# Kernel tuning notes

Measured on AMD Instinct MI355X. Metric: run time of the kernel, lower is better.

## Reference

```python
import jax, jax.numpy as jnp
import numpy as np

B, T, C, H = 4, 2048, 1024, 16
HD = C // H


def setup_inputs() -> dict:
    key = jax.random.key(0)
    k1, k2, k3, k4 = jax.random.split(key, 4)
    x = jax.random.normal(k1, (B, T, C), dtype=jnp.float32)
    pad_mask = jnp.ones((B, T), dtype=jnp.int32)
    # Linear weights stored as (in, out); torch Linear uses W.T so math is identical.
    w_attn = jax.random.normal(k2, (C, 3 * C), dtype=jnp.float32) * (1.0 / np.sqrt(C))
    w_proj = jax.random.normal(k3, (C, C), dtype=jnp.float32) * (1.0 / np.sqrt(C))
    b_proj = jax.random.normal(k4, (C,), dtype=jnp.float32) * 0.01
    return {"x": x, "pad_mask": pad_mask, "w_attn": w_attn, "w_proj": w_proj, "b_proj": b_proj}


def reference(x, pad_mask, w_attn, w_proj, b_proj):
    Bx, Tx, Cx = x.shape
    hd = Cx // H
    qkv = x @ w_attn                                  # (B,T,3C)
    q, k, v = jnp.split(qkv, 3, axis=2)
    # (B,T,C) -> (B,H,T,hd)
    q = q.reshape(Bx, Tx, H, hd).transpose(0, 2, 1, 3)
    k = k.reshape(Bx, Tx, H, hd).transpose(0, 2, 1, 3)
    v = v.reshape(Bx, Tx, H, hd).transpose(0, 2, 1, 3)
    att = jnp.einsum('bhqd,bhkd->bhqk', q, k) * (1.0 / np.sqrt(hd))
    causal = jnp.tril(jnp.ones((Tx, Tx), dtype=bool))[None, None]       # (1,1,T,T)
    keep = causal & (pad_mask[:, None, None, :] != 0)                   # (B,1,T,T) broadcast
    att = jnp.where(keep, att, -jnp.inf)
    att = jax.nn.softmax(att, axis=-1)
    # dropout p=0.0 (eval) -> identity
    y = jnp.einsum('bhqk,bhkd->bhqd', att, v)
    y = y.transpose(0, 2, 1, 3).reshape(Bx, Tx, Cx)
    return y @ w_proj + b_proj
```

## Files before the change

kernel.cpp:

```cpp
#include <hip/hip_runtime.h>
#include <hip/hip_bf16.h>


using short8  = __attribute__((ext_vector_type(8))) short;
using float4_ = __attribute__((ext_vector_type(4))) float;

#define Bb   4
#define Tt   2048
#define Cc   1024
#define Hh   16
#define HDd  64

__device__ __forceinline__ float bf2f(unsigned short u) {
    union { float f; unsigned int i; } x; x.i = ((unsigned int)u) << 16; return x.f;
}
__device__ __forceinline__ unsigned short f2bf(float f) {
    union { float f; unsigned int i; } x; x.f = f;
    unsigned int r = x.i + 0x7fff + ((x.i >> 16) & 1);
    return (unsigned short)(r >> 16);
}
__device__ __forceinline__ float4_ bmfma(short8 a, short8 b, float4_ c) {
    return __builtin_amdgcn_mfma_f32_16x16x32_bf16(a, b, c, 0, 0, 0);
}
__device__ __forceinline__ void gl2lds16(const unsigned short* g, unsigned short* l) {
    __builtin_amdgcn_global_load_lds(
        (const __attribute__((address_space(1))) void*)g,
        (__attribute__((address_space(3))) void*)l, 16, 0, 0);
}

__global__ __launch_bounds__(256) void convert_f32_bf16(
    const float* __restrict__ in, unsigned short* __restrict__ out)
{
    size_t idx = ((size_t)blockIdx.x * 256 + threadIdx.x) * 8;
    float4_ f0 = *(const float4_*)&in[idx];
    float4_ f1 = *(const float4_*)&in[idx + 4];
    short8 h;
    h[0] = (short)f2bf(f0[0]); h[1] = (short)f2bf(f0[1]);
    h[2] = (short)f2bf(f0[2]); h[3] = (short)f2bf(f0[3]);
    h[4] = (short)f2bf(f1[0]); h[5] = (short)f2bf(f1[1]);
    h[6] = (short)f2bf(f1[2]); h[7] = (short)f2bf(f1[3]);
    *(short8*)&out[idx] = h;
}

__global__ __launch_bounds__(256) void transpose_f32_bf16(
    const float* __restrict__ in, unsigned short* __restrict__ out,
    int R, int Ccols)
{
    __shared__ unsigned short tile[32][33];
    int c0 = blockIdx.x * 32, r0 = blockIdx.y * 32;
    int tx = threadIdx.x & 31, ty = threadIdx.x >> 5;
    for (int o = 0; o < 32; o += 8)
        tile[ty + o][tx] = f2bf(in[(size_t)(r0 + ty + o) * Ccols + c0 + tx]);
    __syncthreads();
    for (int o = 0; o < 32; o += 8)
        out[(size_t)(c0 + ty + o) * R + r0 + tx] = tile[tx][ty + o];
}

#define GBK 64

__device__ __forceinline__ void gemm128_main(
    const unsigned short* __restrict__ A, const unsigned short* __restrict__ Bt,
    int K, int m0, int n0,
    unsigned short* As, unsigned short* Bs, float4_ acc[4][4])
{
    int tid  = threadIdx.x;
    int wave = tid >> 6, lane = tid & 63;
    int wm = (wave >> 1) * 64, wn = (wave & 1) * 64;
    int lr = lane & 15, lg = lane >> 4;
    int srow = tid >> 3;
    int scol = (tid & 7) * 8;

    for (int k0 = 0; k0 < K; k0 += GBK) {
        #pragma unroll
        for (int j = 0; j < 4; j++) {
            int row = j * 32 + srow;
            gl2lds16(&A [(size_t)(m0 + row) * K + k0 + scol], &As[row * GBK + scol]);
            gl2lds16(&Bt[(size_t)(n0 + row) * K + k0 + scol], &Bs[row * GBK + scol]);
        }
        __syncthreads();
        #pragma unroll
        for (int ks = 0; ks < GBK; ks += 32) {
            short8 af[4], bf[4];
            #pragma unroll
            for (int i = 0; i < 4; i++) {
                af[i] = *(const short8*)&As[(wm + i * 16 + lr) * GBK + ks + lg * 8];
                bf[i] = *(const short8*)&Bs[(wn + i * 16 + lr) * GBK + ks + lg * 8];
            }
            #pragma unroll
            for (int i = 0; i < 4; i++)
                #pragma unroll
                for (int j = 0; j < 4; j++)
                    acc[i][j] = bmfma(af[i], bf[j], acc[i][j]);
        }
        __syncthreads();
    }
}

__global__ __launch_bounds__(256) void gemm_qkv(
    const unsigned short* __restrict__ A,
    const unsigned short* __restrict__ Bt,
    unsigned short* __restrict__ Q,
    unsigned short* __restrict__ Ko,
    unsigned short* __restrict__ V)
{
    __shared__ unsigned short As[128 * GBK];
    __shared__ unsigned short Bs[128 * GBK];
    int m0 = blockIdx.x * 128, n0 = blockIdx.y * 128;
    float4_ acc[4][4] = {};
    gemm128_main(A, Bt, 1024, m0, n0, As, Bs, acc);

    int lane = threadIdx.x & 63, wave = threadIdx.x >> 6;
    int wm = (wave >> 1) * 64, wn = (wave & 1) * 64;
    int lr = lane & 15, lg = lane >> 4;
    #pragma unroll
    for (int i = 0; i < 4; i++)
        #pragma unroll
        for (int j = 0; j < 4; j++) {
            int n = n0 + wn + 16 * j + lr;
            int which = n >> 10;
            int c = n & 1023;
            int h = c >> 6, d = c & 63;
            unsigned short* dst = (which == 0) ? Q : ((which == 1) ? Ko : V);
            float sc2 = (which == 0) ? 0.125f : 1.0f;
            #pragma unroll
            for (int r = 0; r < 4; r++) {
                int m = m0 + wm + 16 * i + lg * 4 + r;
                int b = m >> 11, t = m & 2047;
                dst[(((size_t)(b * Hh + h) * Tt) + t) * HDd + d] = f2bf(acc[i][j][r] * sc2);
            }
        }
}

__global__ __launch_bounds__(256) void gemm_proj(
    const unsigned short* __restrict__ A,
    const unsigned short* __restrict__ Bt,
    const float* __restrict__ bias,
    float* __restrict__ Out)
{
    __shared__ unsigned short As[128 * GBK];
    __shared__ unsigned short Bs[128 * GBK];
    int m0 = blockIdx.x * 128, n0 = blockIdx.y * 128;
    float4_ acc[4][4] = {};
    gemm128_main(A, Bt, 1024, m0, n0, As, Bs, acc);

    int lane = threadIdx.x & 63, wave = threadIdx.x >> 6;
    int wm = (wave >> 1) * 64, wn = (wave & 1) * 64;
    int lr = lane & 15, lg = lane >> 4;
    #pragma unroll
    for (int i = 0; i < 4; i++)
        #pragma unroll
        for (int j = 0; j < 4; j++) {
            int n = n0 + wn + 16 * j + lr;
            float bv = bias[n];
            #pragma unroll
            for (int r = 0; r < 4; r++) {
                int m = m0 + wm + 16 * i + lg * 4 + r;
                Out[(size_t)m * 1024 + n] = acc[i][j][r] + bv;
            }
        }
}

#define DPAD 72

__global__ __launch_bounds__(256) void attn_fwd(
    const unsigned short* __restrict__ Q,
    const unsigned short* __restrict__ Kg,
    const unsigned short* __restrict__ Vg,
    const int* __restrict__ pad,
    unsigned short* __restrict__ Y)
{
    __shared__ unsigned short smem[128 * DPAD];
    unsigned short* Kt = smem;
    unsigned short* Vt = smem + 64 * DPAD;

    int flat = blockIdx.x;
    int qb = 31 - (flat >> 6);
    int bh = flat & 63;
    int b  = bh >> 4, h = bh & 15;
    const size_t base = (size_t)bh * Tt * HDd;
    int tid  = threadIdx.x;
    int wave = tid >> 6, lane = tid & 63;
    int lr = lane & 15, lg = lane >> 4;
    int q0 = qb * 64 + wave * 16;
    unsigned short* Pw = &Kt[wave * 16 * DPAD];
    const int* padRow = pad + b * Tt;

    short8 qf0 = *(const short8*)&Q[base + (size_t)(q0 + lr) * HDd + lg * 8];
    short8 qf1 = *(const short8*)&Q[base + (size_t)(q0 + lr) * HDd + 32 + lg * 8];

    float m_i[4], l_i[4];
    float4_ o_acc[4];
    #pragma unroll
    for (int r = 0; r < 4; r++) { m_i[r] = -1e30f; l_i[r] = 0.f; }
    #pragma unroll
    for (int dt = 0; dt < 4; dt++) o_acc[dt] = (float4_){0.f, 0.f, 0.f, 0.f};

    for (int kt = 0; kt <= qb; kt++) {
        int k0 = kt * 64;
        {
            int r = tid >> 2, cbase = (tid & 3) * 8;
            #pragma unroll
            for (int half = 0; half < 2; half++) {
                int c = cbase + half * 32;
                *(short8*)&Kt[r * DPAD + c] =
                    *(const short8*)&Kg[base + (size_t)(k0 + r) * HDd + c];
                alignas(16) unsigned short tmp[8];
                *(short8*)tmp = *(const short8*)&Vg[base + (size_t)(k0 + r) * HDd + c];
                #pragma unroll
                for (int j = 0; j < 8; j++) {
                    int d = c + j;
                    Vt[d * DPAD + ((((r >> 3) ^ (d >> 3)) << 3) | (r & 7))] = tmp[j];
                }
            }
        }
        __syncthreads();

        float4_ s[4];
        #pragma unroll
        for (int nt = 0; nt < 4; nt++) {
            short8 kf0 = *(const short8*)&Kt[(nt * 16 + lr) * DPAD + lg * 8];
            short8 kf1 = *(const short8*)&Kt[(nt * 16 + lr) * DPAD + 32 + lg * 8];
            float4_ a = (float4_){0.f, 0.f, 0.f, 0.f};
            a = bmfma(qf0, kf0, a);
            a = bmfma(qf1, kf1, a);
            s[nt] = a;
        }
        #pragma unroll
        for (int nt = 0; nt < 4; nt++) {
            int key = k0 + nt * 16 + lr;
            bool keep_k = padRow[key] != 0;
            #pragma unroll
            for (int r = 0; r < 4; r++) {
                int qrow = q0 + lg * 4 + r;
                float sv = s[nt][r];
                if (!keep_k || key > qrow) sv = -1e30f;
                s[nt][r] = sv;
            }
        }
        float mn[4], alpha[4];
        #pragma unroll
        for (int r = 0; r < 4; r++) {
            float v = fmaxf(fmaxf(s[0][r], s[1][r]), fmaxf(s[2][r], s[3][r]));
            #pragma unroll
            for (int off = 1; off < 16; off <<= 1)
                v = fmaxf(v, __shfl_xor(v, off, 64));
            float m_new = fmaxf(m_i[r], v);
            alpha[r] = __expf(m_i[r] - m_new);
            mn[r] = m_new;
        }
        float rsum[4] = {0.f, 0.f, 0.f, 0.f};
        #pragma unroll
        for (int nt = 0; nt < 4; nt++)
            #pragma unroll
            for (int r = 0; r < 4; r++) {
                float p = __expf(s[nt][r] - mn[r]);
                s[nt][r] = p;
                rsum[r] += p;
            }
        #pragma unroll
        for (int r = 0; r < 4; r++) {
            float v = rsum[r];
            #pragma unroll
            for (int off = 1; off < 16; off <<= 1)
                v += __shfl_xor(v, off, 64);
            l_i[r] = l_i[r] * alpha[r] + v;
            m_i[r] = mn[r];
        }

        __syncthreads();

        #pragma unroll
        for (int nt = 0; nt < 4; nt++)
            #pragma unroll
            for (int r = 0; r < 4; r++)
                Pw[(lg * 4 + r) * DPAD + nt * 16 + lr] = f2bf(s[nt][r]);
        #pragma unroll
        for (int dt = 0; dt < 4; dt++)
            #pragma unroll
            for (int r = 0; r < 4; r++)
                o_acc[dt][r] *= alpha[r];
        short8 pf0 = *(const short8*)&Pw[lr * DPAD + lg * 8];
        short8 pf1 = *(const short8*)&Pw[lr * DPAD + 32 + lg * 8];
        #pragma unroll
        for (int dt = 0; dt < 4; dt++) {
            int d = dt * 16 + lr;
            short8 vf0 = *(const short8*)&Vt[d * DPAD + ((lg ^ (d >> 3)) << 3)];
            short8 vf1 = *(const short8*)&Vt[d * DPAD + (((lg + 4) ^ (d >> 3)) << 3)];
            o_acc[dt] = bmfma(pf0, vf0, o_acc[dt]);
            o_acc[dt] = bmfma(pf1, vf1, o_acc[dt]);
        }
        __syncthreads();
    }

    #pragma unroll
    for (int dt = 0; dt < 4; dt++)
        #pragma unroll
        for (int r = 0; r < 4; r++) {
            int qrow = q0 + lg * 4 + r;
            Y[((size_t)b * Tt + qrow) * Cc + h * HDd + dt * 16 + lr] =
                f2bf(o_acc[dt][r] / l_i[r]);
        }
}

extern "C" void kernel_launch(void* const* d_in, const int* in_sizes, int n_in,
                              void* d_out, int out_size, void* d_ws, size_t ws_size,
                              hipStream_t stream)
{
    const float* x      = (const float*)d_in[0];
    const int*   pad    = (const int*)d_in[1];
    const float* w_attn = (const float*)d_in[2];
    const float* w_proj = (const float*)d_in[3];
    const float* b_proj = (const float*)d_in[4];
    float*       out    = (float*)d_out;

    unsigned short* Wta = (unsigned short*)d_ws;
    unsigned short* Wtp = Wta + (size_t)3072 * 1024;
    unsigned short* Xb  = Wtp + (size_t)1024 * 1024;
    unsigned short* Yb  = Xb;
    unsigned short* Qb  = Xb + (size_t)8192 * 1024;
    unsigned short* Kb  = Qb + (size_t)Bb * Hh * Tt * HDd;
    unsigned short* Vb  = Kb + (size_t)Bb * Hh * Tt * HDd;

    convert_f32_bf16<<<dim3(4096), 256, 0, stream>>>(x, Xb);
    transpose_f32_bf16<<<dim3(3072 / 32, 1024 / 32), 256, 0, stream>>>(w_attn, Wta, 1024, 3072);
    transpose_f32_bf16<<<dim3(1024 / 32, 1024 / 32), 256, 0, stream>>>(w_proj, Wtp, 1024, 1024);
    gemm_qkv<<<dim3(8192 / 128, 3072 / 128), 256, 0, stream>>>(Xb, Wta, Qb, Kb, Vb);
    attn_fwd<<<dim3(2048), 256, 0, stream>>>(Qb, Kb, Vb, pad, Yb);
    gemm_proj<<<dim3(8192 / 128, 1024 / 128), 256, 0, stream>>>(Yb, Wtp, b_proj, out);
}
```

Measured before the change: 331.5 us.

## Pair causal query blocks per workgroup, use exp2 softmax, skip interior masking

```diff
diff --git a/kernel.cpp b/kernel.cpp
--- a/kernel.cpp
+++ b/kernel.cpp
@@ -10,6 +10,8 @@
 #define Cc   1024
 #define Hh   16
 #define HDd  64
+
+#define EXP2F(x) __builtin_amdgcn_exp2f(x)
 
 __device__ __forceinline__ float bf2f(unsigned short u) {
     union { float f; unsigned int i; } x; x.i = ((unsigned int)u) << 16; return x.f;
@@ -96,6 +98,8 @@
     }
 }
 
+#define QSCALE 0.180336879f
+
 __global__ __launch_bounds__(256) void gemm_qkv(
     const unsigned short* __restrict__ A,
     const unsigned short* __restrict__ Bt,
@@ -121,7 +125,7 @@
             int c = n & 1023;
             int h = c >> 6, d = c & 63;
             unsigned short* dst = (which == 0) ? Q : ((which == 1) ? Ko : V);
-            float sc2 = (which == 0) ? 0.125f : 1.0f;
+            float sc2 = (which == 0) ? QSCALE : 1.0f;
             #pragma unroll
             for (int r = 0; r < 4; r++) {
                 int m = m0 + wm + 16 * i + lg * 4 + r;
@@ -162,40 +166,131 @@
 
 #define DPAD 72
 
-__global__ __launch_bounds__(256) void attn_fwd(
+#define ATTN_TILE(q0X, qX0, qX1, mX, lX, oX)                                   \
+    {                                                                          \
+        float4_ s[4];                                                          \
+        _Pragma("unroll")                                                      \
+        for (int nt = 0; nt < 4; nt++) {                                       \
+            short8 kf0 = *(const short8*)&Kt[(nt * 16 + lr) * DPAD + lg * 8];  \
+            short8 kf1 = *(const short8*)&Kt[(nt * 16 + lr) * DPAD + 32 + lg * 8]; \
+            float4_ a = (float4_){0.f, 0.f, 0.f, 0.f};                         \
+            a = bmfma(qX0, kf0, a);                                            \
+            a = bmfma(qX1, kf1, a);                                            \
+            s[nt] = a;                                                         \
+        }                                                                      \
+        bool interior = (k0 + 63 <= (q0X));                                    \
+        if (interior) {                                                        \
+            _Pragma("unroll")                                                  \
+            for (int nt = 0; nt < 4; nt++) {                                   \
+                _Pragma("unroll")                                              \
+                for (int r = 0; r < 4; r++) s[nt][r] += pmask[nt];             \
+            }                                                                  \
+        } else {                                                               \
+            _Pragma("unroll")                                                  \
+            for (int nt = 0; nt < 4; nt++) {                                   \
+                int key = k0 + nt * 16 + lr;                                   \
+                _Pragma("unroll")                                              \
+                for (int r = 0; r < 4; r++) {                                  \
+                    int qrow = (q0X) + lg * 4 + r;                             \
+                    float sv = s[nt][r] + pmask[nt];                           \
+                    if (key > qrow) sv = -1e30f;                               \
+                    s[nt][r] = sv;                                             \
+                }                                                              \
+            }                                                                  \
+        }                                                                      \
+        float mn[4], alpha[4];                                                 \
+        _Pragma("unroll")                                                      \
+        for (int r = 0; r < 4; r++) {                                          \
+            float v = fmaxf(fmaxf(s[0][r], s[1][r]), fmaxf(s[2][r], s[3][r])); \
+            _Pragma("unroll")                                                  \
+            for (int off = 1; off < 16; off <<= 1)                             \
+                v = fmaxf(v, __shfl_xor(v, off, 64));                          \
+            float m_new = fmaxf(mX[r], v);                                     \
+            alpha[r] = EXP2F(mX[r] - m_new);                                   \
+            mn[r] = m_new;                                                     \
+        }                                                                      \
+        float rsum[4] = {0.f, 0.f, 0.f, 0.f};                                  \
+        _Pragma("unroll")                                                      \
+        for (int nt = 0; nt < 4; nt++)                                         \
+            _Pragma("unroll")                                                  \
+            for (int r = 0; r < 4; r++) {                                      \
+                float p = EXP2F(s[nt][r] - mn[r]);                             \
+                s[nt][r] = p;                                                  \
+                rsum[r] += p;                                                  \
+            }                                                                  \
+        _Pragma("unroll")                                                      \
+        for (int r = 0; r < 4; r++) {                                          \
+            float v = rsum[r];                                                 \
+            _Pragma("unroll")                                                  \
+            for (int off = 1; off < 16; off <<= 1)                             \
+                v += __shfl_xor(v, off, 64);                                   \
+            lX[r] = lX[r] * alpha[r] + v;                                      \
+            mX[r] = mn[r];                                                     \
+        }                                                                      \
+        _Pragma("unroll")                                                      \
+        for (int nt = 0; nt < 4; nt++)                                         \
+            _Pragma("unroll")                                                  \
+            for (int r = 0; r < 4; r++)                                        \
+                Pw[(lg * 4 + r) * DPAD + nt * 16 + lr] = f2bf(s[nt][r]);       \
+        _Pragma("unroll")                                                      \
+        for (int dt = 0; dt < 4; dt++)                                         \
+            _Pragma("unroll")                                                  \
+            for (int r = 0; r < 4; r++)                                        \
+                oX[dt][r] *= alpha[r];                                         \
+        short8 pf0 = *(const short8*)&Pw[lr * DPAD + lg * 8];                  \
+        short8 pf1 = *(const short8*)&Pw[lr * DPAD + 32 + lg * 8];             \
+        _Pragma("unroll")                                                      \
+        for (int dt = 0; dt < 4; dt++) {                                       \
+            int d = dt * 16 + lr;                                              \
+            short8 vf0 = *(const short8*)&Vt[d * DPAD + ((lg ^ (d >> 3)) << 3)];       \
+            short8 vf1 = *(const short8*)&Vt[d * DPAD + (((lg + 4) ^ (d >> 3)) << 3)]; \
+            oX[dt] = bmfma(pf0, vf0, oX[dt]);                                  \
+            oX[dt] = bmfma(pf1, vf1, oX[dt]);                                  \
+        }                                                                      \
+    }
+
+__global__ __launch_bounds__(256, 4) void attn_fwd(
     const unsigned short* __restrict__ Q,
     const unsigned short* __restrict__ Kg,
     const unsigned short* __restrict__ Vg,
     const int* __restrict__ pad,
     unsigned short* __restrict__ Y)
 {
-    __shared__ unsigned short smem[128 * DPAD];
+    __shared__ unsigned short smem[192 * DPAD];
     unsigned short* Kt = smem;
     unsigned short* Vt = smem + 64 * DPAD;
-
-    int flat = blockIdx.x;
-    int qb = 31 - (flat >> 6);
-    int bh = flat & 63;
+    unsigned short* Pl = smem + 128 * DPAD;
+
+    int qpair = blockIdx.x;
+    int bh = blockIdx.y;
     int b  = bh >> 4, h = bh & 15;
     const size_t base = (size_t)bh * Tt * HDd;
     int tid  = threadIdx.x;
     int wave = tid >> 6, lane = tid & 63;
     int lr = lane & 15, lg = lane >> 4;
-    int q0 = qb * 64 + wave * 16;
-    unsigned short* Pw = &Kt[wave * 16 * DPAD];
+    unsigned short* Pw = &Pl[wave * 16 * DPAD];
     const int* padRow = pad + b * Tt;
 
-    short8 qf0 = *(const short8*)&Q[base + (size_t)(q0 + lr) * HDd + lg * 8];
-    short8 qf1 = *(const short8*)&Q[base + (size_t)(q0 + lr) * HDd + 32 + lg * 8];
-
-    float m_i[4], l_i[4];
-    float4_ o_acc[4];
-    #pragma unroll
-    for (int r = 0; r < 4; r++) { m_i[r] = -1e30f; l_i[r] = 0.f; }
-    #pragma unroll
-    for (int dt = 0; dt < 4; dt++) o_acc[dt] = (float4_){0.f, 0.f, 0.f, 0.f};
-
-    for (int kt = 0; kt <= qb; kt++) {
+    int qbA = qpair, qbB = 31 - qpair;
+    int q0A = qbA * 64 + wave * 16;
+    int q0B = qbB * 64 + wave * 16;
+
+    short8 qfA0 = *(const short8*)&Q[base + (size_t)(q0A + lr) * HDd + lg * 8];
+    short8 qfA1 = *(const short8*)&Q[base + (size_t)(q0A + lr) * HDd + 32 + lg * 8];
+    short8 qfB0 = *(const short8*)&Q[base + (size_t)(q0B + lr) * HDd + lg * 8];
+    short8 qfB1 = *(const short8*)&Q[base + (size_t)(q0B + lr) * HDd + 32 + lg * 8];
+
+    float mA[4], lA[4], mB[4], lB[4];
+    float4_ oA[4], oB[4];
+    #pragma unroll
+    for (int r = 0; r < 4; r++) { mA[r] = -1e30f; lA[r] = 0.f; mB[r] = -1e30f; lB[r] = 0.f; }
+    #pragma unroll
+    for (int dt = 0; dt < 4; dt++) {
+        oA[dt] = (float4_){0.f, 0.f, 0.f, 0.f};
+        oB[dt] = (float4_){0.f, 0.f, 0.f, 0.f};
+    }
+
+    for (int kt = 0; kt <= qbB; kt++) {
         int k0 = kt * 64;
         {
             int r = tid >> 2, cbase = (tid & 3) * 8;
@@ -215,80 +310,15 @@
         }
         __syncthreads();
 
-        float4_ s[4];
-        #pragma unroll
-        for (int nt = 0; nt < 4; nt++) {
-            short8 kf0 = *(const short8*)&Kt[(nt * 16 + lr) * DPAD + lg * 8];
-            short8 kf1 = *(const short8*)&Kt[(nt * 16 + lr) * DPAD + 32 + lg * 8];
-            float4_ a = (float4_){0.f, 0.f, 0.f, 0.f};
-            a = bmfma(qf0, kf0, a);
-            a = bmfma(qf1, kf1, a);
-            s[nt] = a;
-        }
-        #pragma unroll
-        for (int nt = 0; nt < 4; nt++) {
-            int key = k0 + nt * 16 + lr;
-            bool keep_k = padRow[key] != 0;
-            #pragma unroll
-            for (int r = 0; r < 4; r++) {
-                int qrow = q0 + lg * 4 + r;
-                float sv = s[nt][r];
-                if (!keep_k || key > qrow) sv = -1e30f;
-                s[nt][r] = sv;
-            }
-        }
-        float mn[4], alpha[4];
-        #pragma unroll
-        for (int r = 0; r < 4; r++) {
-            float v = fmaxf(fmaxf(s[0][r], s[1][r]), fmaxf(s[2][r], s[3][r]));
-            #pragma unroll
-            for (int off = 1; off < 16; off <<= 1)
-                v = fmaxf(v, __shfl_xor(v, off, 64));
-            float m_new = fmaxf(m_i[r], v);
-            alpha[r] = __expf(m_i[r] - m_new);
-            mn[r] = m_new;
-        }
-        float rsum[4] = {0.f, 0.f, 0.f, 0.f};
+        float pmask[4];
         #pragma unroll
         for (int nt = 0; nt < 4; nt++)
-            #pragma unroll
-            for (int r = 0; r < 4; r++) {
-                float p = __expf(s[nt][r] - mn[r]);
-                s[nt][r] = p;
-                rsum[r] += p;
-            }
-        #pragma unroll
-        for (int r = 0; r < 4; r++) {
-            float v = rsum[r];
-            #pragma unroll
-            for (int off = 1; off < 16; off <<= 1)
-                v += __shfl_xor(v, off, 64);
-            l_i[r] = l_i[r] * alpha[r] + v;
-            m_i[r] = mn[r];
-        }
-
-        __syncthreads();
-
-        #pragma unroll
-        for (int nt = 0; nt < 4; nt++)
-            #pragma unroll
-            for (int r = 0; r < 4; r++)
-                Pw[(lg * 4 + r) * DPAD + nt * 16 + lr] = f2bf(s[nt][r]);
-        #pragma unroll
-        for (int dt = 0; dt < 4; dt++)
-            #pragma unroll
-            for (int r = 0; r < 4; r++)
-                o_acc[dt][r] *= alpha[r];
-        short8 pf0 = *(const short8*)&Pw[lr * DPAD + lg * 8];
-        short8 pf1 = *(const short8*)&Pw[lr * DPAD + 32 + lg * 8];
-        #pragma unroll
-        for (int dt = 0; dt < 4; dt++) {
-            int d = dt * 16 + lr;
-            short8 vf0 = *(const short8*)&Vt[d * DPAD + ((lg ^ (d >> 3)) << 3)];
-            short8 vf1 = *(const short8*)&Vt[d * DPAD + (((lg + 4) ^ (d >> 3)) << 3)];
-            o_acc[dt] = bmfma(pf0, vf0, o_acc[dt]);
-            o_acc[dt] = bmfma(pf1, vf1, o_acc[dt]);
-        }
+            pmask[nt] = (padRow[k0 + nt * 16 + lr] != 0) ? 0.f : -1e30f;
+
+        ATTN_TILE(q0B, qfB0, qfB1, mB, lB, oB);
+        if (kt <= qbA)
+            ATTN_TILE(q0A, qfA0, qfA1, mA, lA, oA);
+
         __syncthreads();
     }
 
@@ -296,9 +326,10 @@
     for (int dt = 0; dt < 4; dt++)
         #pragma unroll
         for (int r = 0; r < 4; r++) {
-            int qrow = q0 + lg * 4 + r;
-            Y[((size_t)b * Tt + qrow) * Cc + h * HDd + dt * 16 + lr] =
-                f2bf(o_acc[dt][r] / l_i[r]);
+            int qrowA = q0A + lg * 4 + r;
+            int qrowB = q0B + lg * 4 + r;
+            Y[((size_t)b * Tt + qrowA) * Cc + h * HDd + dt * 16 + lr] = f2bf(oA[dt][r] / lA[r]);
+            Y[((size_t)b * Tt + qrowB) * Cc + h * HDd + dt * 16 + lr] = f2bf(oB[dt][r] / lB[r]);
         }
 }
 
@@ -325,6 +356,6 @@
     transpose_f32_bf16<<<dim3(3072 / 32, 1024 / 32), 256, 0, stream>>>(w_attn, Wta, 1024, 3072);
     transpose_f32_bf16<<<dim3(1024 / 32, 1024 / 32), 256, 0, stream>>>(w_proj, Wtp, 1024, 1024);
     gemm_qkv<<<dim3(8192 / 128, 3072 / 128), 256, 0, stream>>>(Xb, Wta, Qb, Kb, Vb);
-    attn_fwd<<<dim3(2048), 256, 0, stream>>>(Qb, Kb, Vb, pad, Yb);
+    attn_fwd<<<dim3(16, Bb * Hh), 256, 0, stream>>>(Qb, Kb, Vb, pad, Yb);
     gemm_proj<<<dim3(8192 / 128, 1024 / 128), 256, 0, stream>>>(Yb, Wtp, b_proj, out);
 }
```

Measured after the change: 359.6 us. 1.08x slower.

## Pair causal query blocks per workgroup, use exp2 softmax, skip mask on full tiles

Applied to the files above, without the earlier changes.

```diff
diff --git a/kernel.cpp b/kernel.cpp
--- a/kernel.cpp
+++ b/kernel.cpp
@@ -10,6 +10,8 @@
 #define Cc   1024
 #define Hh   16
 #define HDd  64
+
+#define EXP2F(x) __builtin_amdgcn_exp2f(x)
 
 __device__ __forceinline__ float bf2f(unsigned short u) {
     union { float f; unsigned int i; } x; x.i = ((unsigned int)u) << 16; return x.f;
@@ -96,6 +98,8 @@
     }
 }
 
+#define QSCALE 0.180336879f
+
 __global__ __launch_bounds__(256) void gemm_qkv(
     const unsigned short* __restrict__ A,
     const unsigned short* __restrict__ Bt,
@@ -121,7 +125,7 @@
             int c = n & 1023;
             int h = c >> 6, d = c & 63;
             unsigned short* dst = (which == 0) ? Q : ((which == 1) ? Ko : V);
-            float sc2 = (which == 0) ? 0.125f : 1.0f;
+            float sc2 = (which == 0) ? QSCALE : 1.0f;
             #pragma unroll
             for (int r = 0; r < 4; r++) {
                 int m = m0 + wm + 16 * i + lg * 4 + r;
@@ -173,133 +177,149 @@
     unsigned short* Kt = smem;
     unsigned short* Vt = smem + 64 * DPAD;
 
-    int flat = blockIdx.x;
-    int qb = 31 - (flat >> 6);
-    int bh = flat & 63;
+    int qpair = blockIdx.x;
+    int bh = blockIdx.y;
     int b  = bh >> 4, h = bh & 15;
     const size_t base = (size_t)bh * Tt * HDd;
     int tid  = threadIdx.x;
     int wave = tid >> 6, lane = tid & 63;
     int lr = lane & 15, lg = lane >> 4;
-    int q0 = qb * 64 + wave * 16;
     unsigned short* Pw = &Kt[wave * 16 * DPAD];
     const int* padRow = pad + b * Tt;
 
-    short8 qf0 = *(const short8*)&Q[base + (size_t)(q0 + lr) * HDd + lg * 8];
-    short8 qf1 = *(const short8*)&Q[base + (size_t)(q0 + lr) * HDd + 32 + lg * 8];
-
-    float m_i[4], l_i[4];
-    float4_ o_acc[4];
-    #pragma unroll
-    for (int r = 0; r < 4; r++) { m_i[r] = -1e30f; l_i[r] = 0.f; }
-    #pragma unroll
-    for (int dt = 0; dt < 4; dt++) o_acc[dt] = (float4_){0.f, 0.f, 0.f, 0.f};
-
-    for (int kt = 0; kt <= qb; kt++) {
-        int k0 = kt * 64;
-        {
-            int r = tid >> 2, cbase = (tid & 3) * 8;
-            #pragma unroll
-            for (int half = 0; half < 2; half++) {
-                int c = cbase + half * 32;
-                *(short8*)&Kt[r * DPAD + c] =
-                    *(const short8*)&Kg[base + (size_t)(k0 + r) * HDd + c];
-                alignas(16) unsigned short tmp[8];
-                *(short8*)tmp = *(const short8*)&Vg[base + (size_t)(k0 + r) * HDd + c];
-                #pragma unroll
-                for (int j = 0; j < 8; j++) {
-                    int d = c + j;
-                    Vt[d * DPAD + ((((r >> 3) ^ (d >> 3)) << 3) | (r & 7))] = tmp[j];
+    for (int ph = 0; ph < 2; ph++) {
+        int qb = ph ? (31 - qpair) : qpair;
+        int q0 = qb * 64 + wave * 16;
+
+        short8 qf0 = *(const short8*)&Q[base + (size_t)(q0 + lr) * HDd + lg * 8];
+        short8 qf1 = *(const short8*)&Q[base + (size_t)(q0 + lr) * HDd + 32 + lg * 8];
+
+        float m_i[4], l_i[4];
+        float4_ o_acc[4];
+        #pragma unroll
+        for (int r = 0; r < 4; r++) { m_i[r] = -1e30f; l_i[r] = 0.f; }
+        #pragma unroll
+        for (int dt = 0; dt < 4; dt++) o_acc[dt] = (float4_){0.f, 0.f, 0.f, 0.f};
+
+        for (int kt = 0; kt <= qb; kt++) {
+            int k0 = kt * 64;
+            {
+                int r = tid >> 2, cbase = (tid & 3) * 8;
+                #pragma unroll
+                for (int half = 0; half < 2; half++) {
+                    int c = cbase + half * 32;
+                    *(short8*)&Kt[r * DPAD + c] =
+                        *(const short8*)&Kg[base + (size_t)(k0 + r) * HDd + c];
+                    alignas(16) unsigned short tmp[8];
+                    *(short8*)tmp = *(const short8*)&Vg[base + (size_t)(k0 + r) * HDd + c];
+                    #pragma unroll
+                    for (int j = 0; j < 8; j++) {
+                        int d = c + j;
+                        Vt[d * DPAD + ((((r >> 3) ^ (d >> 3)) << 3) | (r & 7))] = tmp[j];
+                    }
                 }
             }
-        }
-        __syncthreads();
-
-        float4_ s[4];
-        #pragma unroll
-        for (int nt = 0; nt < 4; nt++) {
-            short8 kf0 = *(const short8*)&Kt[(nt * 16 + lr) * DPAD + lg * 8];
-            short8 kf1 = *(const short8*)&Kt[(nt * 16 + lr) * DPAD + 32 + lg * 8];
-            float4_ a = (float4_){0.f, 0.f, 0.f, 0.f};
-            a = bmfma(qf0, kf0, a);
-            a = bmfma(qf1, kf1, a);
-            s[nt] = a;
-        }
-        #pragma unroll
-        for (int nt = 0; nt < 4; nt++) {
-            int key = k0 + nt * 16 + lr;
-            bool keep_k = padRow[key] != 0;
+            __syncthreads();
+
+            float pmask[4];
+            #pragma unroll
+            for (int nt = 0; nt < 4; nt++)
+                pmask[nt] = (padRow[k0 + nt * 16 + lr] != 0) ? 0.f : -1e30f;
+
+            float4_ s[4];
+            #pragma unroll
+            for (int nt = 0; nt < 4; nt++) {
+                short8 kf0 = *(const short8*)&Kt[(nt * 16 + lr) * DPAD + lg * 8];
+                short8 kf1 = *(const short8*)&Kt[(nt * 16 + lr) * DPAD + 32 + lg * 8];
+                float4_ a = (float4_){0.f, 0.f, 0.f, 0.f};
+                a = bmfma(qf0, kf0, a);
+                a = bmfma(qf1, kf1, a);
+                s[nt] = a;
+            }
+            if (k0 + 63 <= q0) {
+                #pragma unroll
+                for (int nt = 0; nt < 4; nt++)
+                    #pragma unroll
+                    for (int r = 0; r < 4; r++)
+                        s[nt][r] += pmask[nt];
+            } else {
+                #pragma unroll
+                for (int nt = 0; nt < 4; nt++) {
+                    int key = k0 + nt * 16 + lr;
+                    #pragma unroll
+                    for (int r = 0; r < 4; r++) {
+                        int qrow = q0 + lg * 4 + r;
+                        float sv = s[nt][r] + pmask[nt];
+                        if (key > qrow) sv = -1e30f;
+                        s[nt][r] = sv;
+                    }
+                }
+            }
+            float mn[4], alpha[4];
+            #pragma unroll
+            for (int r = 0; r < 4; r++) {
+                float v = fmaxf(fmaxf(s[0][r], s[1][r]), fmaxf(s[2][r], s[3][r]));
+                #pragma unroll
+                for (int off = 1; off < 16; off <<= 1)
+                    v = fmaxf(v, __shfl_xor(v, off, 64));
+                float m_new = fmaxf(m_i[r], v);
+                alpha[r] = EXP2F(m_i[r] - m_new);
+                mn[r] = m_new;
+            }
+            float rsum[4] = {0.f, 0.f, 0.f, 0.f};
+            #pragma unroll
+            for (int nt = 0; nt < 4; nt++)
+                #pragma unroll
+                for (int r = 0; r < 4; r++) {
+                    float p = EXP2F(s[nt][r] - mn[r]);
+                    s[nt][r] = p;
+                    rsum[r] += p;
+                }
+            #pragma unroll
+            for (int r = 0; r < 4; r++) {
+                float v = rsum[r];
+                #pragma unroll
+                for (int off = 1; off < 16; off <<= 1)
+                    v += __shfl_xor(v, off, 64);
+                l_i[r] = l_i[r] * alpha[r] + v;
+                m_i[r] = mn[r];
+            }
+
+            __syncthreads();
+
+            #pragma unroll
+            for (int nt = 0; nt < 4; nt++)
+                #pragma unroll
+                for (int r = 0; r < 4; r++)
+                    Pw[(lg * 4 + r) * DPAD + nt * 16 + lr] = f2bf(s[nt][r]);
+            #pragma unroll
+            for (int dt = 0; dt < 4; dt++)
+                #pragma unroll
+                for (int r = 0; r < 4; r++)
+                    o_acc[dt][r] *= alpha[r];
+            short8 pf0 = *(const short8*)&Pw[lr * DPAD + lg * 8];
+            short8 pf1 = *(const short8*)&Pw[lr * DPAD + 32 + lg * 8];
+            #pragma unroll
+            for (int dt = 0; dt < 4; dt++) {
+                int d = dt * 16 + lr;
+                short8 vf0 = *(const short8*)&Vt[d * DPAD + ((lg ^ (d >> 3)) << 3)];
+                short8 vf1 = *(const short8*)&Vt[d * DPAD + (((lg + 4) ^ (d >> 3)) << 3)];
+                o_acc[dt] = bmfma(pf0, vf0, o_acc[dt]);
+                o_acc[dt] = bmfma(pf1, vf1, o_acc[dt]);
+            }
+            __syncthreads();
+        }
+
+        #pragma unroll
+        for (int dt = 0; dt < 4; dt++)
             #pragma unroll
             for (int r = 0; r < 4; r++) {
                 int qrow = q0 + lg * 4 + r;
-                float sv = s[nt][r];
-                if (!keep_k || key > qrow) sv = -1e30f;
-                s[nt][r] = sv;
-            }
-        }
-        float mn[4], alpha[4];
-        #pragma unroll
-        for (int r = 0; r < 4; r++) {
-            float v = fmaxf(fmaxf(s[0][r], s[1][r]), fmaxf(s[2][r], s[3][r]));
-            #pragma unroll
-            for (int off = 1; off < 16; off <<= 1)
-                v = fmaxf(v, __shfl_xor(v, off, 64));
-            float m_new = fmaxf(m_i[r], v);
-            alpha[r] = __expf(m_i[r] - m_new);
-            mn[r] = m_new;
-        }
-        float rsum[4] = {0.f, 0.f, 0.f, 0.f};
-        #pragma unroll
-        for (int nt = 0; nt < 4; nt++)
-            #pragma unroll
-            for (int r = 0; r < 4; r++) {
-                float p = __expf(s[nt][r] - mn[r]);
-                s[nt][r] = p;
-                rsum[r] += p;
-            }
-        #pragma unroll
-        for (int r = 0; r < 4; r++) {
-            float v = rsum[r];
-            #pragma unroll
-            for (int off = 1; off < 16; off <<= 1)
-                v += __shfl_xor(v, off, 64);
-            l_i[r] = l_i[r] * alpha[r] + v;
-            m_i[r] = mn[r];
-        }
-
-        __syncthreads();
-
-        #pragma unroll
-        for (int nt = 0; nt < 4; nt++)
-            #pragma unroll
-            for (int r = 0; r < 4; r++)
-                Pw[(lg * 4 + r) * DPAD + nt * 16 + lr] = f2bf(s[nt][r]);
-        #pragma unroll
-        for (int dt = 0; dt < 4; dt++)
-            #pragma unroll
-            for (int r = 0; r < 4; r++)
-                o_acc[dt][r] *= alpha[r];
-        short8 pf0 = *(const short8*)&Pw[lr * DPAD + lg * 8];
-        short8 pf1 = *(const short8*)&Pw[lr * DPAD + 32 + lg * 8];
-        #pragma unroll
-        for (int dt = 0; dt < 4; dt++) {
-            int d = dt * 16 + lr;
-            short8 vf0 = *(const short8*)&Vt[d * DPAD + ((lg ^ (d >> 3)) << 3)];
-            short8 vf1 = *(const short8*)&Vt[d * DPAD + (((lg + 4) ^ (d >> 3)) << 3)];
-            o_acc[dt] = bmfma(pf0, vf0, o_acc[dt]);
-            o_acc[dt] = bmfma(pf1, vf1, o_acc[dt]);
-        }
+                Y[((size_t)b * Tt + qrow) * Cc + h * HDd + dt * 16 + lr] =
+                    f2bf(o_acc[dt][r] / l_i[r]);
+            }
         __syncthreads();
     }
-
-    #pragma unroll
-    for (int dt = 0; dt < 4; dt++)
-        #pragma unroll
-        for (int r = 0; r < 4; r++) {
-            int qrow = q0 + lg * 4 + r;
-            Y[((size_t)b * Tt + qrow) * Cc + h * HDd + dt * 16 + lr] =
-                f2bf(o_acc[dt][r] / l_i[r]);
-        }
 }
 
 extern "C" void kernel_launch(void* const* d_in, const int* in_sizes, int n_in,
@@ -325,6 +345,6 @@
     transpose_f32_bf16<<<dim3(3072 / 32, 1024 / 32), 256, 0, stream>>>(w_attn, Wta, 1024, 3072);
     transpose_f32_bf16<<<dim3(1024 / 32, 1024 / 32), 256, 0, stream>>>(w_proj, Wtp, 1024, 1024);
     gemm_qkv<<<dim3(8192 / 128, 3072 / 128), 256, 0, stream>>>(Xb, Wta, Qb, Kb, Vb);
-    attn_fwd<<<dim3(2048), 256, 0, stream>>>(Qb, Kb, Vb, pad, Yb);
+    attn_fwd<<<dim3(16, Bb * Hh), 256, 0, stream>>>(Qb, Kb, Vb, pad, Yb);
     gemm_proj<<<dim3(8192 / 128, 1024 / 128), 256, 0, stream>>>(Yb, Wtp, b_proj, out);
 }
```

After: 378.8 us. 14.3% more time.
